# Optimization experiments

Measured on AMD Instinct MI355X. Metric: run time of the kernel, lower is better.

## Reference

```python
import jax, jax.numpy as jnp
import numpy as np


def setup_inputs() -> dict:
    key = jax.random.key(0)
    k1, k2, k3 = jax.random.split(key, 3)
    B, T, S, D = 8, 2048, 2048, 512
    main_input = jax.random.normal(k1, (B, T, D), dtype=jnp.float32)
    attn_input = jax.random.normal(k2, (B, S, D), dtype=jnp.float32)
    # f_input is a torch Linear(D, D): y = x @ W_f.T + b_f
    W_f = jax.random.normal(k3, (D, D), dtype=jnp.float32) * (1.0 / np.sqrt(D))
    b_f = jnp.zeros((D,), dtype=jnp.float32)
    return {"main_input": main_input, "attn_input": attn_input, "W_f": W_f, "b_f": b_f}


def reference(main_input, attn_input, W_f, b_f):
    # keys: f_input applied to each attn word  [B,S,D]
    keys = jnp.einsum("bsd,ed->bse", attn_input, W_f) + b_f
    # scores[b,t,s] = keys[b,s,:] . main_input[b,t,:]
    scores = jnp.einsum("bse,bte->bts", keys, main_input)
    attn = jax.nn.softmax(scores, axis=-1)  # softmax over attn words S
    # weighted sum of RAW attn_input (values are unprojected)
    out = jnp.einsum("bts,bsd->btd", attn, attn_input)
    return out
```

## Files before the change

### kernel.cpp

```cpp
#include <hip/hip_runtime.h>
#include <math.h>

#define B_  8
#define T_  2048
#define S_  2048
#define D_  512

typedef _Float16 half8   __attribute__((ext_vector_type(8)));
typedef _Float16 half4_t __attribute__((ext_vector_type(4)));
typedef float    floatx4 __attribute__((ext_vector_type(4)));

__device__ __forceinline__ floatx4 mfma16(half8 a, half8 b, floatx4 c) {
  return __builtin_amdgcn_mfma_f32_16x16x32_f16(a, b, c, 0, 0, 0);
}

__device__ __forceinline__ void async16(void* lds, const void* g) {
  __builtin_amdgcn_global_load_lds(
      (const __attribute__((address_space(1))) void*)g,
      (__attribute__((address_space(3))) void*)lds, 16, 0, 0);
}

__global__ __launch_bounds__(256) void transpose_cast_kernel(
    const float* __restrict__ attn, _Float16* __restrict__ Vt) {
  __shared__ _Float16 tile[32][33];
  const int tx = threadIdx.x, ty = threadIdx.y;
  const int b = blockIdx.z, s0 = blockIdx.y * 32, d0 = blockIdx.x * 32;
  const float* src = attn + ((size_t)b * S_ + s0) * D_ + d0;
#pragma unroll
  for (int i = 0; i < 4; ++i) {
    int s = ty + i * 8;
    tile[tx][s] = (_Float16)src[(size_t)s * D_ + tx];
  }
  __syncthreads();
  _Float16* dst = Vt + ((size_t)b * D_ + d0) * S_ + s0;
#pragma unroll
  for (int i = 0; i < 4; ++i) {
    int d = ty + i * 8;
    dst[(size_t)d * S_ + tx] = tile[d][tx];
  }
}

__global__ __launch_bounds__(512, 2) void keys_gemm_kernel(
    const float* __restrict__ X, const float* __restrict__ W,
    const float* __restrict__ bias, _Float16* __restrict__ K16) {
  __shared__ alignas(16) _Float16 Xs[128][72];
  __shared__ alignas(16) _Float16 Ws[128][72];
  const int t = threadIdx.x;
  const int wave = t >> 6, lane = t & 63, q = lane >> 4, n = lane & 15;
  const int wm = wave >> 2, wn = wave & 3;
  const int m0 = blockIdx.x * 128, n0 = blockIdx.y * 128;

  floatx4 acc[4][2];
#pragma unroll
  for (int i = 0; i < 4; ++i)
#pragma unroll
    for (int j = 0; j < 2; ++j) {
      floatx4 z = {0.f, 0.f, 0.f, 0.f};
      acc[i][j] = z;
    }

  for (int kc = 0; kc < 8; ++kc) {
    const int k0 = kc * 64;
#pragma unroll
    for (int i = 0; i < 4; ++i) {
      int seg = i * 512 + t;
      int row = seg >> 4, c4 = (seg & 15) * 4;
      floatx4 xv = *(const floatx4*)&X[(size_t)(m0 + row) * D_ + k0 + c4];
      floatx4 wv = *(const floatx4*)&W[(size_t)(n0 + row) * D_ + k0 + c4];
      half4_t xh, wh;
#pragma unroll
      for (int j = 0; j < 4; ++j) { xh[j] = (_Float16)xv[j]; wh[j] = (_Float16)wv[j]; }
      *(half4_t*)&Xs[row][c4] = xh;
      *(half4_t*)&Ws[row][c4] = wh;
    }
    __syncthreads();
#pragma unroll
    for (int kk = 0; kk < 2; ++kk) {
      half8 a[4], bb[2];
#pragma unroll
      for (int mt = 0; mt < 4; ++mt)
        a[mt] = *(const half8*)&Xs[wm * 64 + mt * 16 + n][kk * 32 + q * 8];
#pragma unroll
      for (int nt = 0; nt < 2; ++nt)
        bb[nt] = *(const half8*)&Ws[wn * 32 + nt * 16 + n][kk * 32 + q * 8];
#pragma unroll
      for (int mt = 0; mt < 4; ++mt)
#pragma unroll
        for (int nt = 0; nt < 2; ++nt)
          acc[mt][nt] = mfma16(a[mt], bb[nt], acc[mt][nt]);
    }
    __syncthreads();
  }

#pragma unroll
  for (int nt = 0; nt < 2; ++nt) {
    int col = n0 + wn * 32 + nt * 16 + n;
    float bv = bias[col];
#pragma unroll
    for (int mt = 0; mt < 4; ++mt)
#pragma unroll
      for (int r = 0; r < 4; ++r) {
        int row = m0 + wm * 64 + mt * 16 + q * 4 + r;
        K16[(size_t)row * D_ + col] = (_Float16)(acc[mt][nt][r] + bv);
      }
  }
}

__global__ __launch_bounds__(256, 1) void flash_kernel(
    const float* __restrict__ Qf, const _Float16* __restrict__ K16,
    const _Float16* __restrict__ Vt, float* __restrict__ out) {
  __shared__ _Float16 Klds[2][32][512];
  __shared__ _Float16 Vlds[2][512][32];
  __shared__ _Float16 Pscr[4][16][40];

  const int t = threadIdx.x;
  const int w = t >> 6, lane = t & 63, qd = lane >> 4, n = lane & 15;
  const int n7 = n & 7;
  const int bid = blockIdx.x;
  const int b = bid & 7, t0 = (bid >> 3) * 64;

  const _Float16* Kb = K16 + (size_t)b * S_ * D_;
  const _Float16* Vb = Vt + (size_t)b * D_ * S_;

  const int ksw = lane ^ 0;
  const int vsw = (lane & 3) ^ ((lane >> 3) & 3);
  const int ccV = qd ^ ((n >> 1) & 3);

  half8 qreg[16];
  {
    const float* qrow = Qf + ((size_t)b * T_ + t0 + w * 16 + n) * D_;
#pragma unroll
    for (int kk = 0; kk < 16; ++kk) {
      floatx4 v0 = *(const floatx4*)&qrow[kk * 32 + qd * 8];
      floatx4 v1 = *(const floatx4*)&qrow[kk * 32 + qd * 8 + 4];
      half8 h;
#pragma unroll
      for (int j = 0; j < 4; ++j) { h[j] = (_Float16)v0[j]; h[j + 4] = (_Float16)v1[j]; }
      qreg[kk] = h;
    }
  }

  floatx4 O[33];
#pragma unroll
  for (int ng = 0; ng < 33; ++ng) {
    floatx4 z = {0.f, 0.f, 0.f, 0.f};
    O[ng] = z;
  }
  float m_st[4];
#pragma unroll
  for (int r = 0; r < 4; ++r) m_st[r] = -1e30f;

  half8 ones8;
#pragma unroll
  for (int j = 0; j < 8; ++j) ones8[j] = (_Float16)1.0f;

#pragma unroll
  for (int i = 0; i < 8; ++i) {
    int row = w * 8 + i;
    async16(&Klds[0][row][0], Kb + (size_t)row * D_ + ((lane ^ (row & 7)) * 8));
  }
#pragma unroll
  for (int i = 0; i < 8; ++i) {
    int d0 = (w * 8 + i) * 16;
    async16(&Vlds[0][d0][0], Vb + (size_t)(d0 + (lane >> 2)) * S_ + vsw * 8);
  }
  __syncthreads();

  for (int st = 0; st < S_ / 32; ++st) {
    const int cur = st & 1, nxt = cur ^ 1;
    const int s0 = st * 32;

    if (st < S_ / 32 - 1) {
#pragma unroll
      for (int i = 0; i < 8; ++i) {
        int row = w * 8 + i;
        async16(&Klds[nxt][row][0],
                Kb + (size_t)(s0 + 32 + row) * D_ + ((lane ^ (row & 7)) * 8));
      }
#pragma unroll
      for (int i = 0; i < 8; ++i) {
        int d0 = (w * 8 + i) * 16;
        async16(&Vlds[nxt][d0][0],
                Vb + (size_t)(d0 + (lane >> 2)) * S_ + s0 + 32 + vsw * 8);
      }
    }

    floatx4 Sa0 = {0.f, 0.f, 0.f, 0.f}, Sa1 = Sa0, Sb0 = Sa0, Sb1 = Sa0;
#pragma unroll
    for (int kk = 0; kk < 8; ++kk) {
      int slot = (kk * 4 + qd) ^ n7;
      half8 b0 = *(const half8*)&Klds[cur][n][slot * 8];
      half8 b1 = *(const half8*)&Klds[cur][16 + n][slot * 8];
      Sa0 = mfma16(qreg[kk], b0, Sa0);
      Sa1 = mfma16(qreg[kk], b1, Sa1);
    }
#pragma unroll
    for (int kk = 8; kk < 16; ++kk) {
      int slot = (kk * 4 + qd) ^ n7;
      half8 b0 = *(const half8*)&Klds[cur][n][slot * 8];
      half8 b1 = *(const half8*)&Klds[cur][16 + n][slot * 8];
      Sb0 = mfma16(qreg[kk], b0, Sb0);
      Sb1 = mfma16(qreg[kk], b1, Sb1);
    }
    floatx4 Sc0 = Sa0 + Sb0, Sc1 = Sa1 + Sb1;

    float alpha[4];
#pragma unroll
    for (int r = 0; r < 4; ++r) {
      float v = fmaxf(Sc0[r], Sc1[r]);
      v = fmaxf(v, __shfl_xor(v, 1, 16));
      v = fmaxf(v, __shfl_xor(v, 2, 16));
      v = fmaxf(v, __shfl_xor(v, 4, 16));
      v = fmaxf(v, __shfl_xor(v, 8, 16));
      float mn = fmaxf(m_st[r], v);
      alpha[r] = __expf(m_st[r] - mn);
      m_st[r] = mn;
    }

    bool unchanged = (alpha[0] == 1.f) & (alpha[1] == 1.f) &
                     (alpha[2] == 1.f) & (alpha[3] == 1.f);
    if (!__all(unchanged)) {
#pragma unroll
      for (int ng = 0; ng < 33; ++ng)
#pragma unroll
        for (int r = 0; r < 4; ++r) O[ng][r] *= alpha[r];
    }

#pragma unroll
    for (int r = 0; r < 4; ++r) {
      float p0 = __expf(Sc0[r] - m_st[r]);
      float p1 = __expf(Sc1[r] - m_st[r]);
      Pscr[w][qd * 4 + r][n] = (_Float16)p0;
      Pscr[w][qd * 4 + r][16 + n] = (_Float16)p1;
    }
    half8 av = *(const half8*)&Pscr[w][n][qd * 8];

#pragma unroll
    for (int ng = 0; ng < 32; ++ng) {
      half8 bv = *(const half8*)&Vlds[cur][ng * 16 + n][ccV * 8];
      O[ng] = mfma16(av, bv, O[ng]);
    }
    O[32] = mfma16(av, ones8, O[32]);

    if (st < S_ / 32 - 1) __syncthreads();
  }

  float* ob = out + ((size_t)b * T_ + t0 + w * 16) * D_;
#pragma unroll
  for (int r = 0; r < 4; ++r) {
    float inv = 1.f / O[32][r];
    const size_t rowoff = (size_t)(qd * 4 + r) * D_;
#pragma unroll
    for (int ng = 0; ng < 32; ++ng)
      ob[rowoff + ng * 16 + n] = O[ng][r] * inv;
  }
}

extern "C" void kernel_launch(void* const* d_in, const int* in_sizes, int n_in,
                              void* d_out, int out_size, void* d_ws, size_t ws_size,
                              hipStream_t stream) {
  (void)in_sizes; (void)n_in; (void)out_size; (void)ws_size;
  const float* main_in = (const float*)d_in[0];
  const float* attn_in = (const float*)d_in[1];
  const float* W_f     = (const float*)d_in[2];
  const float* b_f     = (const float*)d_in[3];
  float* out = (float*)d_out;

  _Float16* K16 = (_Float16*)d_ws;
  _Float16* Vt  = K16 + (size_t)B_ * S_ * D_;

  transpose_cast_kernel<<<dim3(D_ / 32, S_ / 32, B_), dim3(32, 8, 1), 0, stream>>>(
      attn_in, Vt);
  keys_gemm_kernel<<<dim3((B_ * S_) / 128, D_ / 128), 512, 0, stream>>>(
      attn_in, W_f, b_f, K16);
  flash_kernel<<<(B_ * T_) / 64, 256, 0, stream>>>(main_in, K16, Vt, out);
}
```

Measured before the change: 312.6 us.

## Split flash attention work across wave pairs per row group with LDS max exchange

```diff
diff --git a/kernel.cpp b/kernel.cpp
--- a/kernel.cpp
+++ b/kernel.cpp
@@ -18,6 +18,13 @@
   __builtin_amdgcn_global_load_lds(
       (const __attribute__((address_space(1))) void*)g,
       (__attribute__((address_space(3))) void*)lds, 16, 0, 0);
+}
+
+__device__ __forceinline__ void bar_lds() {
+  __builtin_amdgcn_sched_barrier(0);
+  asm volatile("s_waitcnt lgkmcnt(0)" ::: "memory");
+  __builtin_amdgcn_s_barrier();
+  __builtin_amdgcn_sched_barrier(0);
 }
 
 __global__ __launch_bounds__(256) void transpose_cast_kernel(
@@ -106,43 +113,44 @@
   }
 }
 
-__global__ __launch_bounds__(256, 1) void flash_kernel(
+__global__ __launch_bounds__(512, 2) void flash_kernel(
     const float* __restrict__ Qf, const _Float16* __restrict__ K16,
     const _Float16* __restrict__ Vt, float* __restrict__ out) {
-  __shared__ _Float16 Klds[2][32][512];
-  __shared__ _Float16 Vlds[2][512][32];
-  __shared__ _Float16 Pscr[4][16][40];
+  __shared__ alignas(16) _Float16 Klds[2][32][512];
+  __shared__ alignas(16) _Float16 Vlds[2][512][32];
+  __shared__ alignas(16) _Float16 Pscr[4][16][40];
+  __shared__ float Mscr[4][2][16];
 
   const int t = threadIdx.x;
   const int w = t >> 6, lane = t & 63, qd = lane >> 4, n = lane & 15;
   const int n7 = n & 7;
+  const int rg = w >> 1, h = w & 1;
   const int bid = blockIdx.x;
   const int b = bid & 7, t0 = (bid >> 3) * 64;
 
   const _Float16* Kb = K16 + (size_t)b * S_ * D_;
   const _Float16* Vb = Vt + (size_t)b * D_ * S_;
 
-  const int ksw = lane ^ 0;
   const int vsw = (lane & 3) ^ ((lane >> 3) & 3);
   const int ccV = qd ^ ((n >> 1) & 3);
 
   half8 qreg[16];
   {
-    const float* qrow = Qf + ((size_t)b * T_ + t0 + w * 16 + n) * D_;
+    const float* qrow = Qf + ((size_t)b * T_ + t0 + rg * 16 + n) * D_;
 #pragma unroll
     for (int kk = 0; kk < 16; ++kk) {
       floatx4 v0 = *(const floatx4*)&qrow[kk * 32 + qd * 8];
       floatx4 v1 = *(const floatx4*)&qrow[kk * 32 + qd * 8 + 4];
-      half8 h;
-#pragma unroll
-      for (int j = 0; j < 4; ++j) { h[j] = (_Float16)v0[j]; h[j + 4] = (_Float16)v1[j]; }
-      qreg[kk] = h;
-    }
-  }
-
-  floatx4 O[33];
-#pragma unroll
-  for (int ng = 0; ng < 33; ++ng) {
+      half8 hv;
+#pragma unroll
+      for (int j = 0; j < 4; ++j) { hv[j] = (_Float16)v0[j]; hv[j + 4] = (_Float16)v1[j]; }
+      qreg[kk] = hv;
+    }
+  }
+
+  floatx4 O[17];
+#pragma unroll
+  for (int ng = 0; ng < 17; ++ng) {
     floatx4 z = {0.f, 0.f, 0.f, 0.f};
     O[ng] = z;
   }
@@ -155,13 +163,13 @@
   for (int j = 0; j < 8; ++j) ones8[j] = (_Float16)1.0f;
 
 #pragma unroll
-  for (int i = 0; i < 8; ++i) {
-    int row = w * 8 + i;
+  for (int i = 0; i < 4; ++i) {
+    int row = w * 4 + i;
     async16(&Klds[0][row][0], Kb + (size_t)row * D_ + ((lane ^ (row & 7)) * 8));
   }
 #pragma unroll
-  for (int i = 0; i < 8; ++i) {
-    int d0 = (w * 8 + i) * 16;
+  for (int i = 0; i < 4; ++i) {
+    int d0 = (w * 4 + i) * 16;
     async16(&Vlds[0][d0][0], Vb + (size_t)(d0 + (lane >> 2)) * S_ + vsw * 8);
   }
   __syncthreads();
@@ -172,86 +180,89 @@
 
     if (st < S_ / 32 - 1) {
 #pragma unroll
-      for (int i = 0; i < 8; ++i) {
-        int row = w * 8 + i;
+      for (int i = 0; i < 4; ++i) {
+        int row = w * 4 + i;
         async16(&Klds[nxt][row][0],
                 Kb + (size_t)(s0 + 32 + row) * D_ + ((lane ^ (row & 7)) * 8));
       }
 #pragma unroll
-      for (int i = 0; i < 8; ++i) {
-        int d0 = (w * 8 + i) * 16;
+      for (int i = 0; i < 4; ++i) {
+        int d0 = (w * 4 + i) * 16;
         async16(&Vlds[nxt][d0][0],
                 Vb + (size_t)(d0 + (lane >> 2)) * S_ + s0 + 32 + vsw * 8);
       }
     }
 
-    floatx4 Sa0 = {0.f, 0.f, 0.f, 0.f}, Sa1 = Sa0, Sb0 = Sa0, Sb1 = Sa0;
+    floatx4 Sa = {0.f, 0.f, 0.f, 0.f}, Sb = Sa;
 #pragma unroll
     for (int kk = 0; kk < 8; ++kk) {
       int slot = (kk * 4 + qd) ^ n7;
-      half8 b0 = *(const half8*)&Klds[cur][n][slot * 8];
-      half8 b1 = *(const half8*)&Klds[cur][16 + n][slot * 8];
-      Sa0 = mfma16(qreg[kk], b0, Sa0);
-      Sa1 = mfma16(qreg[kk], b1, Sa1);
+      half8 bk = *(const half8*)&Klds[cur][h * 16 + n][slot * 8];
+      Sa = mfma16(qreg[kk], bk, Sa);
     }
 #pragma unroll
     for (int kk = 8; kk < 16; ++kk) {
       int slot = (kk * 4 + qd) ^ n7;
-      half8 b0 = *(const half8*)&Klds[cur][n][slot * 8];
-      half8 b1 = *(const half8*)&Klds[cur][16 + n][slot * 8];
-      Sb0 = mfma16(qreg[kk], b0, Sb0);
-      Sb1 = mfma16(qreg[kk], b1, Sb1);
-    }
-    floatx4 Sc0 = Sa0 + Sb0, Sc1 = Sa1 + Sb1;
-
-    float alpha[4];
+      half8 bk = *(const half8*)&Klds[cur][h * 16 + n][slot * 8];
+      Sb = mfma16(qreg[kk], bk, Sb);
+    }
+    floatx4 Sc = Sa + Sb;
+
 #pragma unroll
     for (int r = 0; r < 4; ++r) {
-      float v = fmaxf(Sc0[r], Sc1[r]);
+      float v = Sc[r];
       v = fmaxf(v, __shfl_xor(v, 1, 16));
       v = fmaxf(v, __shfl_xor(v, 2, 16));
       v = fmaxf(v, __shfl_xor(v, 4, 16));
       v = fmaxf(v, __shfl_xor(v, 8, 16));
-      float mn = fmaxf(m_st[r], v);
+      if (n == qd * 4 + r) Mscr[rg][h][n] = v;
+    }
+    bar_lds();
+
+    float alpha[4];
+#pragma unroll
+    for (int r = 0; r < 4; ++r) {
+      int row = qd * 4 + r;
+      float mt = fmaxf(Mscr[rg][0][row], Mscr[rg][1][row]);
+      float mn = fmaxf(m_st[r], mt);
       alpha[r] = __expf(m_st[r] - mn);
       m_st[r] = mn;
     }
-
     bool unchanged = (alpha[0] == 1.f) & (alpha[1] == 1.f) &
                      (alpha[2] == 1.f) & (alpha[3] == 1.f);
     if (!__all(unchanged)) {
 #pragma unroll
-      for (int ng = 0; ng < 33; ++ng)
+      for (int ng = 0; ng < 17; ++ng)
 #pragma unroll
         for (int r = 0; r < 4; ++r) O[ng][r] *= alpha[r];
     }
 
 #pragma unroll
     for (int r = 0; r < 4; ++r) {
-      float p0 = __expf(Sc0[r] - m_st[r]);
-      float p1 = __expf(Sc1[r] - m_st[r]);
-      Pscr[w][qd * 4 + r][n] = (_Float16)p0;
-      Pscr[w][qd * 4 + r][16 + n] = (_Float16)p1;
-    }
-    half8 av = *(const half8*)&Pscr[w][n][qd * 8];
-
-#pragma unroll
-    for (int ng = 0; ng < 32; ++ng) {
-      half8 bv = *(const half8*)&Vlds[cur][ng * 16 + n][ccV * 8];
+      float p = __expf(Sc[r] - m_st[r]);
+      Pscr[rg][qd * 4 + r][h * 16 + n] = (_Float16)p;
+    }
+    bar_lds();
+
+    half8 av = *(const half8*)&Pscr[rg][n][qd * 8];
+
+#pragma unroll
+    for (int ng = 0; ng < 16; ++ng) {
+      half8 bv = *(const half8*)&Vlds[cur][h * 256 + ng * 16 + n][ccV * 8];
       O[ng] = mfma16(av, bv, O[ng]);
     }
-    O[32] = mfma16(av, ones8, O[32]);
+    O[16] = mfma16(av, ones8, O[16]);
 
     if (st < S_ / 32 - 1) __syncthreads();
   }
 
-  float* ob = out + ((size_t)b * T_ + t0 + w * 16) * D_;
+  float* ob = out + ((size_t)b * T_ + t0 + rg * 16) * D_ + h * 256;
 #pragma unroll
   for (int r = 0; r < 4; ++r) {
-    float inv = 1.f / O[32][r];
+    float inv = 1.f / O[16][r];
     const size_t rowoff = (size_t)(qd * 4 + r) * D_;
 #pragma unroll
-    for (int ng = 0; ng < 32; ++ng)
+    for (int ng = 0; ng < 16; ++ng)
       ob[rowoff + ng * 16 + n] = O[ng][r] * inv;
   }
 }
@@ -273,5 +284,5 @@
       attn_in, Vt);
   keys_gemm_kernel<<<dim3((B_ * S_) / 128, D_ / 128), 512, 0, stream>>>(
       attn_in, W_f, b_f, K16);
-  flash_kernel<<<(B_ * T_) / 64, 256, 0, stream>>>(main_in, K16, Vt, out);
-}
+  flash_kernel<<<(B_ * T_) / 64, 512, 0, stream>>>(main_in, K16, Vt, out);
+}
```

Result: faster. 293.5 us (-6.1%).
